# Kernel tuning notes

Hardware: AMD Instinct MI355X
Metric: run time of the kernel (lower is better)

The kernel has to match this reference:

```python
import jax, jax.numpy as jnp
import numpy as np

N = 100000      # nodes
E = 1600000     # edges (avg degree 16)
IN, H, H4, OUT = 2, 128, 32, 64
B = 1000        # batch_size for final view


def setup_inputs() -> dict:
    key = jax.random.key(0)
    ks = jax.random.split(key, 16)
    w = lambda k, s: (jax.random.normal(k, s, jnp.float32) * (1.0 / np.sqrt(s[0])))
    return {
        "x": jax.random.normal(ks[0], (N, IN), jnp.float32),
        "edge_index": jax.random.randint(ks[1], (2, E), 0, N, dtype=jnp.int32),
        "batch_size": B,
        "W1": w(ks[2], (IN, H)),  "b1": jnp.zeros((H,), jnp.float32),
        "W2": w(ks[3], (H, H)),   "b2": jnp.zeros((H,), jnp.float32),
        "W3": w(ks[4], (H, H4)),  "b3": jnp.zeros((H4,), jnp.float32),
        "W4": w(ks[5], (H4, H4)), "b4": jnp.zeros((H4,), jnp.float32),
        "W5": w(ks[6], (H4, OUT)),"b5": jnp.zeros((OUT,), jnp.float32),
        "Wl": w(ks[7], (OUT, 1)), "bl": jnp.zeros((1,), jnp.float32),
    }


def gcn_conv(x, src, dst, W, b, n):
    # PyG GCNConv: add self-loops, symmetric degree normalization, scatter-add.
    h = x @ W  # [N, F]
    deg = jax.ops.segment_sum(jnp.ones(src.shape[0], h.dtype), dst,
                              num_segments=n) + 1.0  # +1 for self-loop
    dinv = jax.lax.rsqrt(deg)  # deg >= 1, no inf
    norm = dinv[src] * dinv[dst]  # [E]
    agg = jax.ops.segment_sum(h[src] * norm[:, None], dst, num_segments=n)
    agg = agg + h * (dinv * dinv)[:, None]  # self-loop contribution
    return agg + b


def reference(x, edge_index, batch_size, W1, b1, W2, b2, W3, b3, W4, b4, W5, b5, Wl, bl):
    x = x.reshape(-1, 2)
    n = x.shape[0]
    src, dst = edge_index[0], edge_index[1]
    for W, b in ((W1, b1), (W2, b2), (W3, b3), (W4, b4), (W5, b5)):
        x = jax.nn.relu(gcn_conv(x, src, dst, W, b, n))
    x = x @ Wl + bl  # [N, 1]
    return x.reshape(batch_size, -1)
```

## Files before the change

### kernel.cpp

```cpp
#include <hip/hip_runtime.h>
#include <math.h>


static inline int cdiv(int a, int b) { return (a + b - 1) / b; }

__global__ void zero_i32(int* __restrict__ p, int n) {
    int i = blockIdx.x * 256 + threadIdx.x;
    if (i < n) p[i] = 0;
}

__global__ void count_kernel(const int* __restrict__ dst, int* __restrict__ cnt, int E) {
    int e = blockIdx.x * 256 + threadIdx.x;
    if (e < E) atomicAdd(&cnt[dst[e]], 1);
}

__global__ void scan1(const int* __restrict__ cnt, int* __restrict__ off,
                      int* __restrict__ bsum, int n) {
    __shared__ int sm[256];
    int i = blockIdx.x * 256 + threadIdx.x;
    int v = (i < n) ? cnt[i] : 0;
    sm[threadIdx.x] = v;
    __syncthreads();
    for (int ofs = 1; ofs < 256; ofs <<= 1) {
        int t = (threadIdx.x >= (unsigned)ofs) ? sm[threadIdx.x - ofs] : 0;
        __syncthreads();
        sm[threadIdx.x] += t;
        __syncthreads();
    }
    if (i < n) off[i] = sm[threadIdx.x];
    if (threadIdx.x == 255) bsum[blockIdx.x] = sm[255];
}

__global__ void scan2(const int* __restrict__ bsum, int* __restrict__ bpre,
                      int nb, int* __restrict__ off, int N, int E) {
    __shared__ int sm[512];
    int t = threadIdx.x;
    sm[t] = (t < nb) ? bsum[t] : 0;
    __syncthreads();
    for (int ofs = 1; ofs < 512; ofs <<= 1) {
        int v = (t >= ofs) ? sm[t - ofs] : 0;
        __syncthreads();
        sm[t] += v;
        __syncthreads();
    }
    if (t < nb) bpre[t] = sm[t] - bsum[t];
    if (t == 0) off[N] = E;
}

__global__ void scan3_fused(const int* __restrict__ cnt, const int* __restrict__ bpre,
                            int* __restrict__ off, int* __restrict__ cursor,
                            const float* __restrict__ x, float* __restrict__ dinv,
                            float* __restrict__ xs, int n) {
    int i = blockIdx.x * 256 + threadIdx.x;
    if (i < n) {
        int c = cnt[i];
        int o = off[i] - c + bpre[blockIdx.x];
        off[i] = o;
        cursor[i] = o;
        float dv = 1.0f / sqrtf((float)c + 1.0f);
        dinv[i] = dv;
        float2 xv = *reinterpret_cast<const float2*>(x + 2 * (size_t)i);
        *reinterpret_cast<float2*>(xs + 2 * (size_t)i) = float2{dv * xv.x, dv * xv.y};
    }
}

__global__ void fill_kernel(const int* __restrict__ src, const int* __restrict__ dst,
                            int* __restrict__ cursor, int* __restrict__ csr, int E) {
    int e = blockIdx.x * 256 + threadIdx.x;
    if (e < E) {
        int p = atomicAdd(&cursor[dst[e]], 1);
        csr[p] = src[e];
    }
}

__global__ __launch_bounds__(256) void agg2_kernel(const float* __restrict__ xs,
                                                   const int* __restrict__ off,
                                                   const int* __restrict__ csr,
                                                   const float* __restrict__ dinv,
                                                   float* __restrict__ out, int n) {
    int v = blockIdx.x * 256 + threadIdx.x;
    if (v >= n) return;
    float a0 = 0.f, a1 = 0.f;
    int e0 = off[v], e1 = off[v + 1];
    for (int e = e0; e < e1; e++) {
        int s = csr[e];
        float2 q = *reinterpret_cast<const float2*>(xs + 2 * (size_t)s);
        a0 += q.x;
        a1 += q.y;
    }
    float dv = dinv[v];
    float2 xv = *reinterpret_cast<const float2*>(xs + 2 * (size_t)v);
    *reinterpret_cast<float2*>(out + 2 * (size_t)v) =
        float2{dv * (a0 + xv.x), dv * (a1 + xv.y)};
}

template <int F, int L, bool BR, bool PS>
__global__ __launch_bounds__(256) void agg_kernel(const float* __restrict__ h,
                                                  const int* __restrict__ off,
                                                  const int* __restrict__ csr,
                                                  const float* __restrict__ dinv,
                                                  const float* __restrict__ bias,
                                                  float* __restrict__ out, int n) {
    static_assert(F == 4 * L, "each lane owns 4 cols");
    constexpr int NPW = 64 / L;
    constexpr int NPB = 4 * NPW;

    int tid = threadIdx.x;
    int wave = tid >> 6;
    int lane = tid & 63;
    int sub = lane / L;
    int sl = lane % L;
    int v = blockIdx.x * NPB + wave * NPW + sub;
    if (v >= n) return;

    int start = off[v];
    int end = off[v + 1];
    int subbase = sub * L;

    float a0 = 0.f, a1 = 0.f, a2 = 0.f, a3 = 0.f;

    for (int base = start; base < end; base += L) {
        int m = end - base;
        if (m > L) m = L;
        int idx = (sl < m) ? csr[base + sl] : 0;
        int i = 0;
        for (; i + 8 <= m; i += 8) {
            float4 hb[8];
#pragma unroll
            for (int u = 0; u < 8; u++) {
                int s = __shfl(idx, subbase + i + u);
                hb[u] = *reinterpret_cast<const float4*>(h + (size_t)s * F + sl * 4);
            }
#pragma unroll
            for (int u = 0; u < 8; u++) {
                a0 += hb[u].x; a1 += hb[u].y; a2 += hb[u].z; a3 += hb[u].w;
            }
        }
        if (i + 4 <= m) {
            float4 hb[4];
#pragma unroll
            for (int u = 0; u < 4; u++) {
                int s = __shfl(idx, subbase + i + u);
                hb[u] = *reinterpret_cast<const float4*>(h + (size_t)s * F + sl * 4);
            }
#pragma unroll
            for (int u = 0; u < 4; u++) {
                a0 += hb[u].x; a1 += hb[u].y; a2 += hb[u].z; a3 += hb[u].w;
            }
            i += 4;
        }
        if (i + 2 <= m) {
            int s0 = __shfl(idx, subbase + i);
            int s1 = __shfl(idx, subbase + i + 1);
            float4 h0 = *reinterpret_cast<const float4*>(h + (size_t)s0 * F + sl * 4);
            float4 h1 = *reinterpret_cast<const float4*>(h + (size_t)s1 * F + sl * 4);
            a0 += h0.x + h1.x; a1 += h0.y + h1.y;
            a2 += h0.z + h1.z; a3 += h0.w + h1.w;
            i += 2;
        }
        if (i < m) {
            int s0 = __shfl(idx, subbase + i);
            float4 h0 = *reinterpret_cast<const float4*>(h + (size_t)s0 * F + sl * 4);
            a0 += h0.x; a1 += h0.y; a2 += h0.z; a3 += h0.w;
        }
    }

    float dv = dinv[v];
    float4 hv = *reinterpret_cast<const float4*>(h + (size_t)v * F + sl * 4);
    float o0 = dv * (a0 + hv.x);
    float o1 = dv * (a1 + hv.y);
    float o2 = dv * (a2 + hv.z);
    float o3 = dv * (a3 + hv.w);
    if constexpr (BR) {
        float4 b = *reinterpret_cast<const float4*>(bias + sl * 4);
        o0 = fmaxf(o0 + b.x, 0.f);
        o1 = fmaxf(o1 + b.y, 0.f);
        o2 = fmaxf(o2 + b.z, 0.f);
        o3 = fmaxf(o3 + b.w, 0.f);
    }
    if constexpr (PS) {
        o0 *= dv; o1 *= dv; o2 *= dv; o3 *= dv;
    }
    *reinterpret_cast<float4*>(out + (size_t)v * F + sl * 4) = float4{o0, o1, o2, o3};
}

template <int K, int F, bool BR, bool PS>
__global__ __launch_bounds__(256, 4) void gemm_tiled(const float* __restrict__ x,
                                                     const float* __restrict__ W,
                                                     const float* __restrict__ bias,
                                                     const float* __restrict__ dinv,
                                                     float* __restrict__ h, int n) {
    constexpr int KC = 16;
    constexpr int KCP = 20;
    constexpr int ROWS = 64;
    constexpr int TPC = F / 4;
    constexpr int RT = 256 / TPC;
    constexpr int RPT = ROWS / RT;
    static_assert(K % KC == 0, "K must be a multiple of 16");

    __shared__ float Ws[KC * F];
    __shared__ float Xs[ROWS * KCP];

    const int tid = threadIdx.x;
    const int cb = (tid % TPC) * 4;
    const int tr = tid / TPC;
    const int row0 = blockIdx.x * ROWS;

    float acc[RPT][4];
#pragma unroll
    for (int r = 0; r < RPT; r++)
#pragma unroll
        for (int j = 0; j < 4; j++) acc[r][j] = 0.f;

#pragma unroll 1
    for (int k0 = 0; k0 < K; k0 += KC) {
        __syncthreads();
        {
            int r = tid >> 2;
            int kk = (tid & 3) * 4;
            int gr = row0 + r;
            float4 v = (gr < n)
                ? *reinterpret_cast<const float4*>(x + (size_t)gr * K + k0 + kk)
                : float4{0.f, 0.f, 0.f, 0.f};
            *reinterpret_cast<float4*>(&Xs[r * KCP + kk]) = v;
        }
        for (int i = tid; i < KC * F / 4; i += 256) {
            *reinterpret_cast<float4*>(&Ws[i * 4]) =
                *reinterpret_cast<const float4*>(W + (size_t)k0 * F + i * 4);
        }
        __syncthreads();

#pragma unroll
        for (int kk4 = 0; kk4 < KC; kk4 += 4) {
            float4 xr[RPT];
#pragma unroll
            for (int r = 0; r < RPT; r++)
                xr[r] = *reinterpret_cast<const float4*>(&Xs[(tr * RPT + r) * KCP + kk4]);
#pragma unroll
            for (int j = 0; j < 4; j++) {
                float4 w = *reinterpret_cast<const float4*>(&Ws[(kk4 + j) * F + cb]);
#pragma unroll
                for (int r = 0; r < RPT; r++) {
                    float xv = (j == 0) ? xr[r].x : (j == 1) ? xr[r].y
                             : (j == 2) ? xr[r].z : xr[r].w;
                    acc[r][0] += xv * w.x;
                    acc[r][1] += xv * w.y;
                    acc[r][2] += xv * w.z;
                    acc[r][3] += xv * w.w;
                }
            }
        }
    }

    float4 b = float4{0.f, 0.f, 0.f, 0.f};
    if constexpr (BR) b = *reinterpret_cast<const float4*>(bias + cb);
#pragma unroll
    for (int r = 0; r < RPT; r++) {
        int row = row0 + tr * RPT + r;
        if (row < n) {
            float o0 = acc[r][0], o1 = acc[r][1], o2 = acc[r][2], o3 = acc[r][3];
            if constexpr (BR) {
                o0 = fmaxf(o0 + b.x, 0.f);
                o1 = fmaxf(o1 + b.y, 0.f);
                o2 = fmaxf(o2 + b.z, 0.f);
                o3 = fmaxf(o3 + b.w, 0.f);
            }
            if constexpr (PS) {
                float dv = dinv[row];
                o0 *= dv; o1 *= dv; o2 *= dv; o3 *= dv;
            }
            *reinterpret_cast<float4*>(&h[(size_t)row * F + cb]) = float4{o0, o1, o2, o3};
        }
    }
}

template <int K, int F, bool BR, bool PS>
__global__ __launch_bounds__(256, 4) void gemm_small(const float* __restrict__ x,
                                                     const float* __restrict__ W,
                                                     const float* __restrict__ bias,
                                                     const float* __restrict__ dinv,
                                                     float* __restrict__ h, int n) {
    constexpr int TPR = F / 4;
    constexpr int ROWS = 256 / TPR;
    __shared__ float Ws[K * F];
    for (int i = threadIdx.x; i < K * F; i += 256) Ws[i] = W[i];
    __syncthreads();

    int tid = threadIdx.x;
    int cb = (tid % TPR) * 4;
    int r = blockIdx.x * ROWS + tid / TPR;
    if (r >= n) return;

    const float* xr = x + (size_t)r * K;
    float a0 = 0.f, a1 = 0.f, a2 = 0.f, a3 = 0.f;
#pragma unroll
    for (int k = 0; k < K; k++) {
        float xv = xr[k];
        float4 w = *reinterpret_cast<const float4*>(&Ws[k * F + cb]);
        a0 += xv * w.x; a1 += xv * w.y; a2 += xv * w.z; a3 += xv * w.w;
    }
    if constexpr (BR) {
        float4 b = *reinterpret_cast<const float4*>(bias + cb);
        a0 = fmaxf(a0 + b.x, 0.f);
        a1 = fmaxf(a1 + b.y, 0.f);
        a2 = fmaxf(a2 + b.z, 0.f);
        a3 = fmaxf(a3 + b.w, 0.f);
    }
    if constexpr (PS) {
        float dv = dinv[r];
        a0 *= dv; a1 *= dv; a2 *= dv; a3 *= dv;
    }
    *reinterpret_cast<float4*>(&h[(size_t)r * F + cb]) = float4{a0, a1, a2, a3};
}

__global__ __launch_bounds__(256) void final_kernel(const float* __restrict__ x,
                                                    const float* __restrict__ Wl,
                                                    const float* __restrict__ bl,
                                                    float* __restrict__ out, int n) {
    __shared__ float w[64];
    if (threadIdx.x < 64) w[threadIdx.x] = Wl[threadIdx.x];
    __syncthreads();
    int i = blockIdx.x * 256 + threadIdx.x;
    if (i >= n) return;
    const float* r = x + (size_t)i * 64;
    float acc = 0.f;
#pragma unroll
    for (int k = 0; k < 64; k += 4) {
        float4 xv = *reinterpret_cast<const float4*>(r + k);
        acc += xv.x * w[k] + xv.y * w[k + 1] + xv.z * w[k + 2] + xv.w * w[k + 3];
    }
    out[i] = acc + bl[0];
}

extern "C" void kernel_launch(void* const* d_in, const int* in_sizes, int n_in,
                              void* d_out, int out_size, void* d_ws, size_t ws_size,
                              hipStream_t stream) {
    const float* x = (const float*)d_in[0];
    const int* ei = (const int*)d_in[1];
    const float* W1 = (const float*)d_in[3];
    const float* b1 = (const float*)d_in[4];
    const float* W2 = (const float*)d_in[5];
    const float* b2 = (const float*)d_in[6];
    const float* W3 = (const float*)d_in[7];
    const float* b3 = (const float*)d_in[8];
    const float* W4 = (const float*)d_in[9];
    const float* b4 = (const float*)d_in[10];
    const float* W5 = (const float*)d_in[11];
    const float* b5 = (const float*)d_in[12];
    const float* Wl = (const float*)d_in[13];
    const float* bl = (const float*)d_in[14];

    const int N = in_sizes[0] / 2;
    const int E = in_sizes[1] / 2;
    const int* src = ei;
    const int* dst = ei + E;

    char* wp = (char*)d_ws;
    auto alloc = [&](size_t bytes) -> void* {
        void* p = wp;
        wp += ((bytes + 255) / 256) * 256;
        return p;
    };
    int* cnt = (int*)alloc((size_t)N * 4);
    int* off = (int*)alloc((size_t)(N + 1) * 4);
    int* cursor = (int*)alloc((size_t)N * 4);
    int* bsum = (int*)alloc(512 * 4);
    int* bpre = (int*)alloc(512 * 4);
    int* csr = (int*)alloc((size_t)E * 4);
    float* dinv = (float*)alloc((size_t)N * 4);
    float* xs2 = (float*)alloc((size_t)N * 2 * 4);
    float* t2 = (float*)alloc((size_t)N * 2 * 4);
    float* bufA = (float*)alloc((size_t)N * 128 * 4);
    float* bufB = (float*)alloc((size_t)N * 128 * 4);

    const int gN = cdiv(N, 256);
    const int gE = cdiv(E, 256);
    const int nb = gN;
    const int gT = cdiv(N, 64);

    zero_i32<<<gN, 256, 0, stream>>>(cnt, N);
    count_kernel<<<gE, 256, 0, stream>>>(dst, cnt, E);
    scan1<<<nb, 256, 0, stream>>>(cnt, off, bsum, N);
    scan2<<<1, 512, 0, stream>>>(bsum, bpre, nb, off, N, E);
    scan3_fused<<<nb, 256, 0, stream>>>(cnt, bpre, off, cursor, x, dinv, xs2, N);
    fill_kernel<<<gE, 256, 0, stream>>>(src, dst, cursor, csr, E);

    agg2_kernel<<<gN, 256, 0, stream>>>(xs2, off, csr, dinv, t2, N);
    gemm_small<2, 128, true, true><<<cdiv(N, 8), 256, 0, stream>>>(t2, W1, b1, dinv, bufA, N);
    gemm_tiled<128, 128, false, false><<<gT, 256, 0, stream>>>(bufA, W2, nullptr, nullptr, bufB, N);
    agg_kernel<128, 32, true, true><<<cdiv(N, 8), 256, 0, stream>>>(bufB, off, csr, dinv, b2, bufA, N);
    gemm_tiled<128, 32, false, false><<<gT, 256, 0, stream>>>(bufA, W3, nullptr, nullptr, bufB, N);
    agg_kernel<32, 8, true, true><<<cdiv(N, 32), 256, 0, stream>>>(bufB, off, csr, dinv, b3, bufA, N);
    gemm_tiled<32, 32, false, false><<<gT, 256, 0, stream>>>(bufA, W4, nullptr, nullptr, bufB, N);
    agg_kernel<32, 8, true, true><<<cdiv(N, 32), 256, 0, stream>>>(bufB, off, csr, dinv, b4, bufA, N);
    agg_kernel<32, 8, false, false><<<cdiv(N, 32), 256, 0, stream>>>(bufA, off, csr, dinv, nullptr, bufB, N);
    gemm_tiled<32, 64, true, false><<<gT, 256, 0, stream>>>(bufB, W5, b5, nullptr, bufA, N);
    final_kernel<<<gN, 256, 0, stream>>>(bufA, Wl, bl, (float*)d_out, N);
}
```

Measured before the change: 627.8 us.

## Partition count and fill atomics by destination range per block class

The edge-count and CSR-fill kernels now launch 8 block classes per edge chunk. Each class scans the whole chunk but performs atomics only for destinations in its eighth of the node range. The intent is to localize atomic traffic (likely to XCD/L2 slices via blockIdx mod 8), cutting cross-die atomic contention. In exchange, dst is read eight times and each thread loops over its chunk.

```diff
diff --git a/kernel.cpp b/kernel.cpp
--- a/kernel.cpp
+++ b/kernel.cpp
@@ -9,9 +9,20 @@
     if (i < n) p[i] = 0;
 }
 
-__global__ void count_kernel(const int* __restrict__ dst, int* __restrict__ cnt, int E) {
-    int e = blockIdx.x * 256 + threadIdx.x;
-    if (e < E) atomicAdd(&cnt[dst[e]], 1);
+__global__ __launch_bounds__(256) void count_ranged(const int* __restrict__ dst,
+                                                    int* __restrict__ cnt,
+                                                    int E, int N, int echunk) {
+    int cls = blockIdx.x & 7;
+    int chunk = blockIdx.x >> 3;
+    int per = (N + 7) >> 3;
+    int lo = cls * per;
+    int hi = lo + per; if (hi > N) hi = N;
+    int e0 = chunk * echunk;
+    int e1 = e0 + echunk; if (e1 > E) e1 = E;
+    for (int e = e0 + (int)threadIdx.x; e < e1; e += 256) {
+        int d = dst[e];
+        if (d >= lo && d < hi) atomicAdd(&cnt[d], 1);
+    }
 }
 
 __global__ void scan1(const int* __restrict__ cnt, int* __restrict__ off,
@@ -64,12 +75,24 @@
     }
 }
 
-__global__ void fill_kernel(const int* __restrict__ src, const int* __restrict__ dst,
-                            int* __restrict__ cursor, int* __restrict__ csr, int E) {
-    int e = blockIdx.x * 256 + threadIdx.x;
-    if (e < E) {
-        int p = atomicAdd(&cursor[dst[e]], 1);
-        csr[p] = src[e];
+__global__ __launch_bounds__(256) void fill_ranged(const int* __restrict__ src,
+                                                   const int* __restrict__ dst,
+                                                   int* __restrict__ cursor,
+                                                   int* __restrict__ csr,
+                                                   int E, int N, int echunk) {
+    int cls = blockIdx.x & 7;
+    int chunk = blockIdx.x >> 3;
+    int per = (N + 7) >> 3;
+    int lo = cls * per;
+    int hi = lo + per; if (hi > N) hi = N;
+    int e0 = chunk * echunk;
+    int e1 = e0 + echunk; if (e1 > E) e1 = E;
+    for (int e = e0 + (int)threadIdx.x; e < e1; e += 256) {
+        int d = dst[e];
+        if (d >= lo && d < hi) {
+            int p = atomicAdd(&cursor[d], 1);
+            csr[p] = src[e];
+        }
     }
 }
 
@@ -374,16 +397,19 @@
     float* bufB = (float*)alloc((size_t)N * 128 * 4);
 
     const int gN = cdiv(N, 256);
-    const int gE = cdiv(E, 256);
     const int nb = gN;
     const int gT = cdiv(N, 64);
 
+    const int NCHUNK = 128;
+    const int echunk = cdiv(E, NCHUNK);
+    const int gR = 8 * NCHUNK;
+
     zero_i32<<<gN, 256, 0, stream>>>(cnt, N);
-    count_kernel<<<gE, 256, 0, stream>>>(dst, cnt, E);
+    count_ranged<<<gR, 256, 0, stream>>>(dst, cnt, E, N, echunk);
     scan1<<<nb, 256, 0, stream>>>(cnt, off, bsum, N);
     scan2<<<1, 512, 0, stream>>>(bsum, bpre, nb, off, N, E);
     scan3_fused<<<nb, 256, 0, stream>>>(cnt, bpre, off, cursor, x, dinv, xs2, N);
-    fill_kernel<<<gE, 256, 0, stream>>>(src, dst, cursor, csr, E);
+    fill_ranged<<<gR, 256, 0, stream>>>(src, dst, cursor, csr, E, N, echunk);
 
     agg2_kernel<<<gN, 256, 0, stream>>>(xs2, off, csr, dinv, t2, N);
     gemm_small<2, 128, true, true><<<cdiv(N, 8), 256, 0, stream>>>(t2, W1, b1, dinv, bufA, N);
```

Result: faster. 580.9 us (-7.5%).
